# Performance work log

Hardware: AMD Instinct MI355X
Metric: run time of the kernel (lower is better)

The kernel has to match this reference:

```python
import jax, jax.numpy as jnp
import numpy as np

D_IN = 1024
D_OUT = 1024
H = 16


def setup_inputs() -> dict:
    key = jax.random.key(0)
    ks = jax.random.split(key, 11)
    B, Tq, Tk = 2, 2048, 2048
    s = 1.0 / np.sqrt(D_IN)
    return {
        "q": jax.random.normal(ks[0], (B, Tq, D_IN), jnp.float32),
        "k": jax.random.normal(ks[1], (B, Tk, D_IN), jnp.float32),
        "v": jax.random.normal(ks[2], (B, Tk, D_IN), jnp.float32),
        "Wq": jax.random.uniform(ks[3], (D_IN, D_OUT), jnp.float32, -s, s),
        "bq": jax.random.uniform(ks[4], (D_OUT,), jnp.float32, -s, s),
        "Wk": jax.random.uniform(ks[5], (D_IN, D_OUT), jnp.float32, -s, s),
        "bk": jax.random.uniform(ks[6], (D_OUT,), jnp.float32, -s, s),
        "Wv": jax.random.uniform(ks[7], (D_IN, D_OUT), jnp.float32, -s, s),
        "bv": jax.random.uniform(ks[8], (D_OUT,), jnp.float32, -s, s),
        "Wo": jax.random.uniform(ks[9], (D_OUT, D_OUT), jnp.float32, -s, s),
        "bo": jax.random.uniform(ks[10], (D_OUT,), jnp.float32, -s, s),
    }


def reference(q, k, v, Wq, bq, Wk, bk, Wv, bv, Wo, bo):
    B, Tq, _ = q.shape
    Tk = k.shape[1]
    hd = D_OUT // H
    # QKV projections, split heads -> [B, H, T, hd]
    qh = (q @ Wq + bq).reshape(B, Tq, H, hd).transpose(0, 2, 1, 3)
    kh = (k @ Wk + bk).reshape(B, Tk, H, hd).transpose(0, 2, 1, 3)
    vh = (v @ Wv + bv).reshape(B, Tk, H, hd).transpose(0, 2, 1, 3)
    # scaled dot-product attention (scale uses key dim = head_dim)
    scores = jnp.einsum("bhqd,bhkd->bhqk", qh, kh) / jnp.sqrt(jnp.float32(hd))
    attn = jax.nn.softmax(scores, axis=-1)
    x = jnp.einsum("bhqk,bhkd->bhqd", attn, vh)
    x = x.transpose(0, 2, 1, 3).reshape(B, Tq, D_OUT)
    return x @ Wo + bo
```

## Files before the change

kernel.cpp:

```cpp
#include <hip/hip_runtime.h>
#include <hip/hip_bf16.h>

typedef __attribute__((ext_vector_type(8))) short short8;
typedef __attribute__((ext_vector_type(4))) short short4v;
typedef __attribute__((ext_vector_type(4))) float f32x4;

__device__ __forceinline__ unsigned short f2bf(float f) {
    __hip_bfloat16 h = __float2bfloat16(f);
    unsigned short u;
    __builtin_memcpy(&u, &h, 2);
    return u;
}
__device__ __forceinline__ short4v pack4bf(float a, float b, float c, float d) {
    union { __hip_bfloat162 h[2]; short4v s; } r;
    r.h[0] = __float22bfloat162_rn(make_float2(a, b));
    r.h[1] = __float22bfloat162_rn(make_float2(c, d));
    return r.s;
}

#define GLD16(gp, lp) __builtin_amdgcn_global_load_lds( \
    (const __attribute__((address_space(1))) void*)(gp), \
    (__attribute__((address_space(3))) void*)(lp), 16, 0, 0)

#define PHASE(WAITN) do { \
        asm volatile("s_waitcnt vmcnt(" #WAITN ")" ::: "memory"); \
        __builtin_amdgcn_s_barrier(); \
        asm volatile("" ::: "memory"); \
        __builtin_amdgcn_sched_barrier(0); } while (0)

__global__ __launch_bounds__(256) void prep(
    const float* __restrict__ q, const float* __restrict__ k, const float* __restrict__ v,
    unsigned short* __restrict__ qb, unsigned short* __restrict__ kb, unsigned short* __restrict__ vb,
    const float* __restrict__ W0, const float* __restrict__ W1,
    const float* __restrict__ W2, const float* __restrict__ W3,
    unsigned short* __restrict__ T0, unsigned short* __restrict__ T1,
    unsigned short* __restrict__ T2, unsigned short* __restrict__ T3)
{
    __shared__ unsigned short Ts[64 * 68];
    int bx = blockIdx.x;
    if (bx < 6144) {
        const float* src; unsigned short* dst;
        switch (bx >> 11) { case 0: src = q; dst = qb; break;
                            case 1: src = k; dst = kb; break;
                            default: src = v; dst = vb; break; }
        size_t i = ((size_t)(bx & 2047) * 256 + threadIdx.x) * 8;
        float4 x0 = *(const float4*)&src[i];
        float4 x1 = *(const float4*)&src[i + 4];
        union { unsigned short s[8]; uint4 u; } p;
        p.s[0] = f2bf(x0.x); p.s[1] = f2bf(x0.y); p.s[2] = f2bf(x0.z); p.s[3] = f2bf(x0.w);
        p.s[4] = f2bf(x1.x); p.s[5] = f2bf(x1.y); p.s[6] = f2bf(x1.z); p.s[7] = f2bf(x1.w);
        *(uint4*)&dst[i] = p.u;
        return;
    }
    int w = bx - 6144;
    int z = w >> 8, rem = w & 255;
    int kx = rem >> 4, ny = rem & 15;
    const float* W;
    unsigned short* T;
    switch (z) {
        case 0: W = W0; T = T0; break;
        case 1: W = W1; T = T1; break;
        case 2: W = W2; T = T2; break;
        default: W = W3; T = T3; break;
    }
    int tid = threadIdx.x;
    int c = tid & 7, r = tid >> 3;
    int k0 = kx * 64, n0 = ny * 64;
    for (int i = 0; i < 64; i += 32) {
        const float* src = &W[(size_t)(k0 + r + i) * 1024 + n0 + c * 8];
        float4 x0 = *(const float4*)src;
        float4 x1 = *(const float4*)(src + 4);
        unsigned short* d = &Ts[(r + i) * 68 + c * 8];
        d[0] = f2bf(x0.x); d[1] = f2bf(x0.y); d[2] = f2bf(x0.z); d[3] = f2bf(x0.w);
        d[4] = f2bf(x1.x); d[5] = f2bf(x1.y); d[6] = f2bf(x1.z); d[7] = f2bf(x1.w);
    }
    __syncthreads();
    for (int i = 0; i < 64; i += 32) {
        union { unsigned short s[8]; uint4 v; } u;
        for (int j = 0; j < 8; j++) u.s[j] = Ts[(c * 8 + j) * 68 + (r + i)];
        *(uint4*)&T[(size_t)(n0 + r + i) * 1024 + k0 + c * 8] = u.v;
    }
}

__device__ __forceinline__ void gemm_core_p(
    const unsigned short* __restrict__ A, const unsigned short* __restrict__ BT,
    const float* __restrict__ bias, unsigned short* __restrict__ out16,
    int mode, float scale)
{
    const int K = 1024;
    __shared__ unsigned short As[3][128 * 32];
    __shared__ unsigned short Bs[3][128 * 32];
    int tid = threadIdx.x;
    int m0 = blockIdx.x * 128, n0 = blockIdx.y * 128;
    int lane = tid & 63, wave = tid >> 6;
    int lm = lane & 15, quad = lane >> 4;
    int wm = (wave >> 1) * 64, wn = (wave & 1) * 64;

    int lrow = lane >> 2;
    int scol = ((lane & 3) ^ ((lane >> 3) & 3)) * 8;
    const unsigned short* Ag = A + (size_t)(m0 + wave * 32 + lrow) * K + scol;
    const unsigned short* Bg = BT + (size_t)(n0 + wave * 32 + lrow) * K + scol;

    int rpos = (quad ^ ((lm >> 1) & 3)) * 8;

    f32x4 acc[4][4];
    for (int i = 0; i < 4; i++)
        for (int j = 0; j < 4; j++)
            for (int r = 0; r < 4; r++) acc[i][j][r] = 0.0f;

#define GSTAGE(BUF) do { \
        GLD16(Ag,          &As[BUF][(wave * 32) * 32]); \
        GLD16(Ag + 16 * K, &As[BUF][(wave * 32 + 16) * 32]); \
        GLD16(Bg,          &Bs[BUF][(wave * 32) * 32]); \
        GLD16(Bg + 16 * K, &Bs[BUF][(wave * 32 + 16) * 32]); \
        Ag += 32; Bg += 32; } while (0)

#define GCOMP(BUF) do { \
        short8 a[4], b[4]; \
        _Pragma("unroll") \
        for (int i = 0; i < 4; i++) \
            a[i] = *(const short8*)&As[BUF][(wm + i * 16 + lm) * 32 + rpos]; \
        _Pragma("unroll") \
        for (int j = 0; j < 4; j++) \
            b[j] = *(const short8*)&Bs[BUF][(wn + j * 16 + lm) * 32 + rpos]; \
        _Pragma("unroll") \
        for (int i = 0; i < 4; i++) \
            _Pragma("unroll") \
            for (int j = 0; j < 4; j++) \
                acc[i][j] = __builtin_amdgcn_mfma_f32_16x16x32_bf16(a[i], b[j], acc[i][j], 0, 0, 0); \
        } while (0)

    GSTAGE(0); GSTAGE(1);
    for (int u = 0; u < 10; u++) {
        PHASE(4); GSTAGE(2); GCOMP(0);
        PHASE(4); GSTAGE(0); GCOMP(1);
        PHASE(4); GSTAGE(1); GCOMP(2);
    }
    PHASE(4); GCOMP(0);
    PHASE(0); GCOMP(1);

#undef GSTAGE
#undef GCOMP

    for (int j = 0; j < 4; j++) {
        int col = n0 + wn + j * 16 + lm;
        float bv = bias[col];
        for (int i = 0; i < 4; i++) {
            int rowb = m0 + wm + i * 16 + quad * 4;
            int h = col >> 6, d = col & 63;
            int bb = rowb >> 11, t = rowb & 2047;
            if (mode == 1) {
                size_t base = (((size_t)(bb * 16 + h)) * 2048 + t) * 64 + d;
                for (int r = 0; r < 4; r++)
                    out16[base + (size_t)r * 64] = f2bf((acc[i][j][r] + bv) * scale);
            } else {
                ushort4 pk;
                pk.x = f2bf((acc[i][j][0] + bv) * scale);
                pk.y = f2bf((acc[i][j][1] + bv) * scale);
                pk.z = f2bf((acc[i][j][2] + bv) * scale);
                pk.w = f2bf((acc[i][j][3] + bv) * scale);
                *(ushort4*)&out16[(((size_t)(bb * 16 + h)) * 64 + d) * 2048 + t] = pk;
            }
        }
    }
}

__global__ __launch_bounds__(256, 3) void qkv_gemm(
    const unsigned short* __restrict__ qbf, const unsigned short* __restrict__ kbf,
    const unsigned short* __restrict__ vbf,
    const unsigned short* __restrict__ WqT, const unsigned short* __restrict__ WkT,
    const unsigned short* __restrict__ WvT,
    const float* __restrict__ bq, const float* __restrict__ bk, const float* __restrict__ bv,
    unsigned short* __restrict__ Qh, unsigned short* __restrict__ Kh,
    unsigned short* __restrict__ VhT)
{
    switch (blockIdx.z) {
        case 0:  gemm_core_p(qbf, WqT, bq, Qh,  1, 0.18033688011f); break;
        case 1:  gemm_core_p(kbf, WkT, bk, Kh,  1, 1.0f);           break;
        default: gemm_core_p(vbf, WvT, bv, VhT, 2, 1.0f);           break;
    }
}

__global__ __launch_bounds__(256, 4) void out_gemm(
    const unsigned short* __restrict__ A, const unsigned short* __restrict__ BT,
    const float* __restrict__ bias, float* __restrict__ out)
{
    const int K = 1024;
    __shared__ unsigned short As[3][64 * 32];
    __shared__ unsigned short Bs[3][64 * 32];
    int tid = threadIdx.x;
    int m0 = blockIdx.x * 64, n0 = blockIdx.y * 64;
    int lane = tid & 63, wave = tid >> 6;
    int lm = lane & 15, quad = lane >> 4;

    int lrow = lane >> 2;
    int scol = ((lane & 3) ^ ((lane >> 3) & 3)) * 8;
    const unsigned short* Ag = A + (size_t)(m0 + wave * 16 + lrow) * K + scol;
    const unsigned short* Bg = BT + (size_t)(n0 + wave * 16 + lrow) * K + scol;

    int rpos = (quad ^ ((lm >> 1) & 3)) * 8;

    f32x4 acc[4];
    for (int j = 0; j < 4; j++)
        for (int r = 0; r < 4; r++) acc[j][r] = 0.0f;

#define OSTAGE(BUF) do { \
        GLD16(Ag, &As[BUF][(wave * 16) * 32]); \
        GLD16(Bg, &Bs[BUF][(wave * 16) * 32]); \
        Ag += 32; Bg += 32; } while (0)

#define OCOMP(BUF) do { \
        short8 a = *(const short8*)&As[BUF][(wave * 16 + lm) * 32 + rpos]; \
        short8 b[4]; \
        _Pragma("unroll") \
        for (int j = 0; j < 4; j++) \
            b[j] = *(const short8*)&Bs[BUF][(j * 16 + lm) * 32 + rpos]; \
        _Pragma("unroll") \
        for (int j = 0; j < 4; j++) \
            acc[j] = __builtin_amdgcn_mfma_f32_16x16x32_bf16(a, b[j], acc[j], 0, 0, 0); \
        } while (0)

    OSTAGE(0); OSTAGE(1);
    for (int u = 0; u < 10; u++) {
        PHASE(2); OSTAGE(2); OCOMP(0);
        PHASE(2); OSTAGE(0); OCOMP(1);
        PHASE(2); OSTAGE(1); OCOMP(2);
    }
    PHASE(2); OCOMP(0);
    PHASE(0); OCOMP(1);

#undef OSTAGE
#undef OCOMP

    for (int j = 0; j < 4; j++) {
        int col = n0 + j * 16 + lm;
        float bv = bias[col];
        int rowb = m0 + wave * 16 + quad * 4;
        for (int r = 0; r < 4; r++)
            out[(size_t)(rowb + r) * 1024 + col] = acc[j][r] + bv;
    }
}

__global__ __launch_bounds__(256) void attn_kernel(
    const unsigned short* __restrict__ Qh, const unsigned short* __restrict__ Kh,
    const unsigned short* __restrict__ VhT, unsigned short* __restrict__ X)
{
    __shared__ unsigned short Ks[4][64 * 64];
    __shared__ unsigned short Vt[4][64 * 64];

    int tid = threadIdx.x;
    int qblk = blockIdx.x & 15, bh = blockIdx.x >> 4;
    int b = bh >> 4, h = bh & 15;
    int lane = tid & 63, wave = tid >> 6;
    int lm = lane & 15, quad = lane >> 4;

    const unsigned short* Kbase = Kh + (size_t)bh * 2048 * 64;
    const unsigned short* Vbase = VhT + (size_t)bh * 64 * 2048;

    int srow = wave * 8 + (lane >> 3);
    int schk = ((lane & 7) ^ ((lane >> 3) & 7)) * 8;
    int swz  = lm & 7;

    const char* ks0 = (const char*)&Ks[0][0] + lm * 128 + ((quad ^ swz) * 16);
    const char* ks1 = (const char*)&Ks[0][0] + lm * 128 + (((quad + 4) ^ swz) * 16);
    int qh2 = quad >> 1, wo = (quad & 1) * 8;
    const char* vt0 = (const char*)&Vt[0][0] + lm * 128 + (((0 + qh2) ^ swz) * 16) + wo;
    const char* vt1 = (const char*)&Vt[0][0] + lm * 128 + (((2 + qh2) ^ swz) * 16) + wo;
    const char* vt2 = (const char*)&Vt[0][0] + lm * 128 + (((4 + qh2) ^ swz) * 16) + wo;
    const char* vt3 = (const char*)&Vt[0][0] + lm * 128 + (((6 + qh2) ^ swz) * 16) + wo;

    const unsigned short* Kg = Kbase + (size_t)srow * 64 + schk;
    const unsigned short* Vg = Vbase + (size_t)srow * 2048 + schk;

    int qrow = qblk * 128 + wave * 32 + lm;
    const unsigned short* qptr = Qh + ((size_t)bh * 2048 + qrow) * 64;
    short8 qfa0 = *(const short8*)&qptr[quad * 8];
    short8 qfa1 = *(const short8*)&qptr[32 + quad * 8];
    short8 qfb0 = *(const short8*)&qptr[16 * 64 + quad * 8];
    short8 qfb1 = *(const short8*)&qptr[16 * 64 + 32 + quad * 8];
    asm volatile("s_waitcnt vmcnt(0)" ::: "memory");

    f32x4 oA[4], oB[4];
    for (int n = 0; n < 4; n++)
        for (int r = 0; r < 4; r++) { oA[n][r] = 0.0f; oB[n][r] = 0.0f; }
    float lA = 0.0f, lB = 0.0f;
    f32x4 zf;
    zf[0] = zf[1] = zf[2] = zf[3] = 0.0f;

#define STAGE(BUF) do { \
        GLD16(Kg,             &Ks[BUF][(wave * 8) * 64]); \
        GLD16(Kg + 32 * 64,   &Ks[BUF][(32 + wave * 8) * 64]); \
        GLD16(Vg,             &Vt[BUF][(wave * 8) * 64]); \
        GLD16(Vg + 32 * 2048, &Vt[BUF][(32 + wave * 8) * 64]); \
        Kg += 64 * 64; Vg += 64; } while (0)

#define QKPV(CUR) do { \
        short4v pa[4], pb[4]; \
        _Pragma("unroll") \
        for (int t = 0; t < 4; t++) { \
            short8 ka0 = *(const short8*)(ks0 + (CUR) * 8192 + t * 2048); \
            short8 ka1 = *(const short8*)(ks1 + (CUR) * 8192 + t * 2048); \
            f32x4 za = __builtin_amdgcn_mfma_f32_16x16x32_bf16(ka0, qfa0, zf, 0, 0, 0); \
            za = __builtin_amdgcn_mfma_f32_16x16x32_bf16(ka1, qfa1, za, 0, 0, 0); \
            f32x4 zb = __builtin_amdgcn_mfma_f32_16x16x32_bf16(ka0, qfb0, zf, 0, 0, 0); \
            zb = __builtin_amdgcn_mfma_f32_16x16x32_bf16(ka1, qfb1, zb, 0, 0, 0); \
            float a0 = __builtin_amdgcn_exp2f(za[0]); \
            float a1 = __builtin_amdgcn_exp2f(za[1]); \
            float a2 = __builtin_amdgcn_exp2f(za[2]); \
            float a3 = __builtin_amdgcn_exp2f(za[3]); \
            lA += (a0 + a1) + (a2 + a3); \
            pa[t] = pack4bf(a0, a1, a2, a3); \
            float b0 = __builtin_amdgcn_exp2f(zb[0]); \
            float b1 = __builtin_amdgcn_exp2f(zb[1]); \
            float b2 = __builtin_amdgcn_exp2f(zb[2]); \
            float b3 = __builtin_amdgcn_exp2f(zb[3]); \
            lB += (b0 + b1) + (b2 + b3); \
            pb[t] = pack4bf(b0, b1, b2, b3); \
        } \
        _Pragma("unroll") \
        for (int n = 0; n < 4; n++) { \
            short4v v0 = *(const short4v*)(vt0 + (CUR) * 8192 + n * 2048); \
            short4v v1 = *(const short4v*)(vt1 + (CUR) * 8192 + n * 2048); \
            short4v v2 = *(const short4v*)(vt2 + (CUR) * 8192 + n * 2048); \
            short4v v3 = *(const short4v*)(vt3 + (CUR) * 8192 + n * 2048); \
            oA[n] = __builtin_amdgcn_mfma_f32_16x16x16bf16_1k(pa[0], v0, oA[n], 0, 0, 0); \
            oB[n] = __builtin_amdgcn_mfma_f32_16x16x16bf16_1k(pb[0], v0, oB[n], 0, 0, 0); \
            oA[n] = __builtin_amdgcn_mfma_f32_16x16x16bf16_1k(pa[1], v1, oA[n], 0, 0, 0); \
            oB[n] = __builtin_amdgcn_mfma_f32_16x16x16bf16_1k(pb[1], v1, oB[n], 0, 0, 0); \
            oA[n] = __builtin_amdgcn_mfma_f32_16x16x16bf16_1k(pa[2], v2, oA[n], 0, 0, 0); \
            oB[n] = __builtin_amdgcn_mfma_f32_16x16x16bf16_1k(pb[2], v2, oB[n], 0, 0, 0); \
            oA[n] = __builtin_amdgcn_mfma_f32_16x16x16bf16_1k(pa[3], v3, oA[n], 0, 0, 0); \
            oB[n] = __builtin_amdgcn_mfma_f32_16x16x16bf16_1k(pb[3], v3, oB[n], 0, 0, 0); \
        } } while (0)

    STAGE(0); STAGE(1); STAGE(2);

    for (int u = 0; u < 7; u++) {
        PHASE(8); STAGE(3); QKPV(0);
        PHASE(8); STAGE(0); QKPV(1);
        PHASE(8); STAGE(1); QKPV(2);
        PHASE(8); STAGE(2); QKPV(3);
    }
    PHASE(8); STAGE(3); QKPV(0);
    PHASE(8); QKPV(1);
    PHASE(4); QKPV(2);
    PHASE(0); QKPV(3);

#undef STAGE
#undef QKPV

    lA += __shfl_xor(lA, 16);
    lA += __shfl_xor(lA, 32);
    lB += __shfl_xor(lB, 16);
    lB += __shfl_xor(lB, 32);
    float invA = 1.0f / lA;
    float invB = 1.0f / lB;

    for (int r = 0; r < 4; r++) {
        int src = (lane & 48) | (quad * 4 + r);
        float invAr = __shfl(invA, src);
        float invBr = __shfl(invB, src);
        int rowA = qblk * 128 + wave * 32 + quad * 4 + r;
        for (int n = 0; n < 4; n++) {
            X[((size_t)b * 2048 + rowA) * 1024 + h * 64 + n * 16 + lm] = f2bf(oA[n][r] * invAr);
            X[((size_t)b * 2048 + rowA + 16) * 1024 + h * 64 + n * 16 + lm] = f2bf(oB[n][r] * invBr);
        }
    }
}

extern "C" void kernel_launch(void* const* d_in, const int* in_sizes, int n_in,
                              void* d_out, int out_size, void* d_ws, size_t ws_size,
                              hipStream_t stream)
{
    const float* q  = (const float*)d_in[0];
    const float* k  = (const float*)d_in[1];
    const float* v  = (const float*)d_in[2];
    const float* Wq = (const float*)d_in[3];
    const float* bq = (const float*)d_in[4];
    const float* Wk = (const float*)d_in[5];
    const float* bk = (const float*)d_in[6];
    const float* Wv = (const float*)d_in[7];
    const float* bv = (const float*)d_in[8];
    const float* Wo = (const float*)d_in[9];
    const float* bo = (const float*)d_in[10];

    unsigned short* ws  = (unsigned short*)d_ws;
    const unsigned int M1 = 1u << 20;
    unsigned short* WqT = ws;
    unsigned short* WkT = ws + M1;
    unsigned short* WvT = ws + 2 * M1;
    unsigned short* WoT = ws + 3 * M1;
    unsigned short* qbf = ws + 4 * M1;
    unsigned short* kbf = ws + 8 * M1;
    unsigned short* vbf = ws + 12 * M1;
    unsigned short* Qh  = ws + 16 * M1;
    unsigned short* Kh  = ws + 4 * M1;
    unsigned short* VhT = ws + 8 * M1;
    unsigned short* X   = ws + 12 * M1;

    prep<<<dim3(7168), 256, 0, stream>>>(q, k, v, qbf, kbf, vbf,
                                         Wq, Wk, Wv, Wo, WqT, WkT, WvT, WoT);
    qkv_gemm<<<dim3(32, 8, 3), 256, 0, stream>>>(qbf, kbf, vbf, WqT, WkT, WvT,
                                                 bq, bk, bv, Qh, Kh, VhT);
    attn_kernel<<<dim3(512), 256, 0, stream>>>(Qh, Kh, VhT, X);
    out_gemm<<<dim3(64, 16), 256, 0, stream>>>(X, WoT, bo, (float*)d_out);
}
```

Before: 220.7 us.

## Fuse fp32-to-bf16 activation conversion into QKV GEMM A-operand loads

Removes the separate prep pass that converted q, k and v to bf16. The QKV GEMM now streams fp32 activations straight into LDS through direct global-to-LDS loads with a new XOR swizzle, then converts them to bf16 when building the MFMA operands. This drops one full write and re-read of the activations, but it doubles the A-tile LDS footprint and global traffic per tile, adds conversion work inside the inner loop, and lowers the occupancy target from 3 to 2 blocks per CU.

```diff
diff --git a/kernel.cpp b/kernel.cpp
--- a/kernel.cpp
+++ b/kernel.cpp
@@ -17,6 +17,7 @@
     r.h[1] = __float22bfloat162_rn(make_float2(c, d));
     return r.s;
 }
+union cat8 { short4v h[2]; short8 v8; };
 
 #define GLD16(gp, lp) __builtin_amdgcn_global_load_lds( \
     (const __attribute__((address_space(1))) void*)(gp), \
@@ -29,30 +30,13 @@
         __builtin_amdgcn_sched_barrier(0); } while (0)
 
 __global__ __launch_bounds__(256) void prep(
-    const float* __restrict__ q, const float* __restrict__ k, const float* __restrict__ v,
-    unsigned short* __restrict__ qb, unsigned short* __restrict__ kb, unsigned short* __restrict__ vb,
     const float* __restrict__ W0, const float* __restrict__ W1,
     const float* __restrict__ W2, const float* __restrict__ W3,
     unsigned short* __restrict__ T0, unsigned short* __restrict__ T1,
     unsigned short* __restrict__ T2, unsigned short* __restrict__ T3)
 {
     __shared__ unsigned short Ts[64 * 68];
-    int bx = blockIdx.x;
-    if (bx < 6144) {
-        const float* src; unsigned short* dst;
-        switch (bx >> 11) { case 0: src = q; dst = qb; break;
-                            case 1: src = k; dst = kb; break;
-                            default: src = v; dst = vb; break; }
-        size_t i = ((size_t)(bx & 2047) * 256 + threadIdx.x) * 8;
-        float4 x0 = *(const float4*)&src[i];
-        float4 x1 = *(const float4*)&src[i + 4];
-        union { unsigned short s[8]; uint4 u; } p;
-        p.s[0] = f2bf(x0.x); p.s[1] = f2bf(x0.y); p.s[2] = f2bf(x0.z); p.s[3] = f2bf(x0.w);
-        p.s[4] = f2bf(x1.x); p.s[5] = f2bf(x1.y); p.s[6] = f2bf(x1.z); p.s[7] = f2bf(x1.w);
-        *(uint4*)&dst[i] = p.u;
-        return;
-    }
-    int w = bx - 6144;
+    int w = blockIdx.x;
     int z = w >> 8, rem = w & 255;
     int kx = rem >> 4, ny = rem & 15;
     const float* W;
@@ -82,13 +66,13 @@
     }
 }
 
-__device__ __forceinline__ void gemm_core_p(
-    const unsigned short* __restrict__ A, const unsigned short* __restrict__ BT,
+__device__ __forceinline__ void gemm_core_f32a(
+    const float* __restrict__ A, const unsigned short* __restrict__ BT,
     const float* __restrict__ bias, unsigned short* __restrict__ out16,
     int mode, float scale)
 {
     const int K = 1024;
-    __shared__ unsigned short As[3][128 * 32];
+    __shared__ float As[3][128 * 32];
     __shared__ unsigned short Bs[3][128 * 32];
     int tid = threadIdx.x;
     int m0 = blockIdx.x * 128, n0 = blockIdx.y * 128;
@@ -96,11 +80,15 @@
     int lm = lane & 15, quad = lane >> 4;
     int wm = (wave >> 1) * 64, wn = (wave & 1) * 64;
 
+    int arow = lane >> 3;
+    int acol = ((lane & 7) ^ arow) * 4;
+    const float* Ag = A + (size_t)(m0 + wave * 32 + arow) * K + acol;
     int lrow = lane >> 2;
     int scol = ((lane & 3) ^ ((lane >> 3) & 3)) * 8;
-    const unsigned short* Ag = A + (size_t)(m0 + wave * 32 + lrow) * K + scol;
     const unsigned short* Bg = BT + (size_t)(n0 + wave * 32 + lrow) * K + scol;
 
+    int pa0 = ((2 * quad) ^ (lm & 7)) * 4;
+    int pa1 = ((2 * quad + 1) ^ (lm & 7)) * 4;
     int rpos = (quad ^ ((lm >> 1) & 3)) * 8;
 
     f32x4 acc[4][4];
@@ -109,17 +97,24 @@
             for (int r = 0; r < 4; r++) acc[i][j][r] = 0.0f;
 
 #define GSTAGE(BUF) do { \
-        GLD16(Ag,          &As[BUF][(wave * 32) * 32]); \
+        GLD16(Ag,          &As[BUF][(wave * 32 +  0) * 32]); \
+        GLD16(Ag +  8 * K, &As[BUF][(wave * 32 +  8) * 32]); \
         GLD16(Ag + 16 * K, &As[BUF][(wave * 32 + 16) * 32]); \
+        GLD16(Ag + 24 * K, &As[BUF][(wave * 32 + 24) * 32]); \
         GLD16(Bg,          &Bs[BUF][(wave * 32) * 32]); \
         GLD16(Bg + 16 * K, &Bs[BUF][(wave * 32 + 16) * 32]); \
         Ag += 32; Bg += 32; } while (0)
 
 #define GCOMP(BUF) do { \
-        short8 a[4], b[4]; \
-        _Pragma("unroll") \
-        for (int i = 0; i < 4; i++) \
-            a[i] = *(const short8*)&As[BUF][(wm + i * 16 + lm) * 32 + rpos]; \
+        cat8 a[4]; short8 b[4]; \
+        _Pragma("unroll") \
+        for (int i = 0; i < 4; i++) { \
+            const float* ar = &As[BUF][(wm + i * 16 + lm) * 32]; \
+            f32x4 af0 = *(const f32x4*)(ar + pa0); \
+            f32x4 af1 = *(const f32x4*)(ar + pa1); \
+            a[i].h[0] = pack4bf(af0[0], af0[1], af0[2], af0[3]); \
+            a[i].h[1] = pack4bf(af1[0], af1[1], af1[2], af1[3]); \
+        } \
         _Pragma("unroll") \
         for (int j = 0; j < 4; j++) \
             b[j] = *(const short8*)&Bs[BUF][(wn + j * 16 + lm) * 32 + rpos]; \
@@ -127,16 +122,16 @@
         for (int i = 0; i < 4; i++) \
             _Pragma("unroll") \
             for (int j = 0; j < 4; j++) \
-                acc[i][j] = __builtin_amdgcn_mfma_f32_16x16x32_bf16(a[i], b[j], acc[i][j], 0, 0, 0); \
+                acc[i][j] = __builtin_amdgcn_mfma_f32_16x16x32_bf16(a[i].v8, b[j], acc[i][j], 0, 0, 0); \
         } while (0)
 
     GSTAGE(0); GSTAGE(1);
     for (int u = 0; u < 10; u++) {
-        PHASE(4); GSTAGE(2); GCOMP(0);
-        PHASE(4); GSTAGE(0); GCOMP(1);
-        PHASE(4); GSTAGE(1); GCOMP(2);
-    }
-    PHASE(4); GCOMP(0);
+        PHASE(6); GSTAGE(2); GCOMP(0);
+        PHASE(6); GSTAGE(0); GCOMP(1);
+        PHASE(6); GSTAGE(1); GCOMP(2);
+    }
+    PHASE(6); GCOMP(0);
     PHASE(0); GCOMP(1);
 
 #undef GSTAGE
@@ -165,9 +160,9 @@
     }
 }
 
-__global__ __launch_bounds__(256, 3) void qkv_gemm(
-    const unsigned short* __restrict__ qbf, const unsigned short* __restrict__ kbf,
-    const unsigned short* __restrict__ vbf,
+__global__ __launch_bounds__(256, 2) void qkv_gemm(
+    const float* __restrict__ q, const float* __restrict__ k,
+    const float* __restrict__ v,
     const unsigned short* __restrict__ WqT, const unsigned short* __restrict__ WkT,
     const unsigned short* __restrict__ WvT,
     const float* __restrict__ bq, const float* __restrict__ bk, const float* __restrict__ bv,
@@ -175,9 +170,9 @@
     unsigned short* __restrict__ VhT)
 {
     switch (blockIdx.z) {
-        case 0:  gemm_core_p(qbf, WqT, bq, Qh,  1, 0.18033688011f); break;
-        case 1:  gemm_core_p(kbf, WkT, bk, Kh,  1, 1.0f);           break;
-        default: gemm_core_p(vbf, WvT, bv, VhT, 2, 1.0f);           break;
+        case 0:  gemm_core_f32a(q, WqT, bq, Qh,  1, 0.18033688011f); break;
+        case 1:  gemm_core_f32a(k, WkT, bk, Kh,  1, 1.0f);           break;
+        default: gemm_core_f32a(v, WvT, bv, VhT, 2, 1.0f);           break;
     }
 }
 
@@ -390,17 +385,13 @@
     unsigned short* WkT = ws + M1;
     unsigned short* WvT = ws + 2 * M1;
     unsigned short* WoT = ws + 3 * M1;
-    unsigned short* qbf = ws + 4 * M1;
-    unsigned short* kbf = ws + 8 * M1;
-    unsigned short* vbf = ws + 12 * M1;
-    unsigned short* Qh  = ws + 16 * M1;
     unsigned short* Kh  = ws + 4 * M1;
     unsigned short* VhT = ws + 8 * M1;
     unsigned short* X   = ws + 12 * M1;
-
-    prep<<<dim3(7168), 256, 0, stream>>>(q, k, v, qbf, kbf, vbf,
-                                         Wq, Wk, Wv, Wo, WqT, WkT, WvT, WoT);
-    qkv_gemm<<<dim3(32, 8, 3), 256, 0, stream>>>(qbf, kbf, vbf, WqT, WkT, WvT,
+    unsigned short* Qh  = ws + 16 * M1;
+
+    prep<<<dim3(1024), 256, 0, stream>>>(Wq, Wk, Wv, Wo, WqT, WkT, WvT, WoT);
+    qkv_gemm<<<dim3(32, 8, 3), 256, 0, stream>>>(q, k, v, WqT, WkT, WvT,
                                                  bq, bk, bv, Qh, Kh, VhT);
     attn_kernel<<<dim3(512), 256, 0, stream>>>(Qh, Kh, VhT, X);
     out_gemm<<<dim3(64, 16), 256, 0, stream>>>(X, WoT, bo, (float*)d_out);
```

Result: slower. 251.6 us (+14.0%).
